# Kernel optimization log

Hardware: AMD Instinct MI355X
Metric: run time of the kernel (lower is better)

Reference implementation:

```python
import jax, jax.numpy as jnp
import numpy as np

EMBED_DIM = 1024
NUM_HEADS = 16
HEAD_DIM = EMBED_DIM // NUM_HEADS


def setup_inputs() -> dict:
    key = jax.random.key(0)
    ks = jax.random.split(key, 10)
    s = 1.0 / np.sqrt(EMBED_DIM)
    x = jax.random.normal(ks[0], (4, 2048, EMBED_DIM), dtype=jnp.float32)
    return {
        "x": x,
        "Wq": jax.random.normal(ks[1], (EMBED_DIM, EMBED_DIM), jnp.float32) * s,
        "bq": jnp.zeros((EMBED_DIM,), jnp.float32),
        "Wk": jax.random.normal(ks[2], (EMBED_DIM, EMBED_DIM), jnp.float32) * s,
        "bk": jnp.zeros((EMBED_DIM,), jnp.float32),
        "Wv": jax.random.normal(ks[3], (EMBED_DIM, EMBED_DIM), jnp.float32) * s,
        "bv": jnp.zeros((EMBED_DIM,), jnp.float32),
        "Wo": jax.random.normal(ks[4], (EMBED_DIM, EMBED_DIM), jnp.float32) * s,
        "bo": jnp.zeros((EMBED_DIM,), jnp.float32),
        "head_scaling": jnp.ones((NUM_HEADS,), jnp.float32),
    }


def reference(x, Wq, bq, Wk, bk, Wv, bv, Wo, bo, head_scaling):
    B, S, E = x.shape
    H, D = NUM_HEADS, HEAD_DIM
    scale = 1.0 / np.sqrt(D)
    # projections (torch Linear: y = x @ W.T + b)
    q = (x @ Wq.T + bq).reshape(B, S, H, D).transpose(0, 2, 1, 3)  # [B,H,S,D]
    k = (x @ Wk.T + bk).reshape(B, S, H, D).transpose(0, 2, 1, 3)
    v = (x @ Wv.T + bv).reshape(B, S, H, D).transpose(0, 2, 1, 3)
    scores = jnp.einsum("bhqd,bhkd->bhqk", q, k) * scale
    attn = jax.nn.softmax(scores, axis=-1)
    head_imp = jax.nn.softmax(head_scaling)[None, :, None, None]  # [1,H,1,1]
    attn = attn * head_imp
    out = jnp.einsum("bhqk,bhkd->bhqd", attn, v)
    out = out.transpose(0, 2, 1, 3).reshape(B, S, E)
    return out @ Wo.T + bo
```

## Files before the change

### kernel.cpp

```cpp
#include <hip/hip_runtime.h>

typedef __bf16 bf16x8 __attribute__((ext_vector_type(8)));
typedef float f32x4 __attribute__((ext_vector_type(4)));
typedef unsigned short ushort8v __attribute__((ext_vector_type(8)));

constexpr int E = 1024;
constexpr int T = 8192;
constexpr size_t TE  = (size_t)T * E;
constexpr size_t WSZ = (size_t)E * E;

#define QSCALE 0.18033688011112042f

__device__ __forceinline__ unsigned short f2bf(float f) {
    union { float f; unsigned int i; } x; x.f = f;
    unsigned int i = x.i;
    return (unsigned short)((i + 0x7fffu + ((i >> 16) & 1u)) >> 16);
}

__device__ __forceinline__ void gload16(const unsigned short* g, unsigned short* l) {
    __builtin_amdgcn_global_load_lds(
        (const __attribute__((address_space(1))) unsigned int*)g,
        (__attribute__((address_space(3))) unsigned int*)l, 16, 0, 0);
}

__global__ __launch_bounds__(256)
void cvt_kernel(const float* __restrict__ x,
                const float* __restrict__ w0, const float* __restrict__ w1,
                const float* __restrict__ w2, const float* __restrict__ w3,
                unsigned short* __restrict__ xb, unsigned short* __restrict__ wb)
{
    size_t i = ((size_t)blockIdx.x * 256 + threadIdx.x) * 8;
    const float* src;
    unsigned short* dst;
    if (i < TE) { src = x + i; dst = xb + i; }
    else {
        size_t j = i - TE;
        int w = (int)(j >> 20);
        size_t off = j & (WSZ - 1);
        src = (w == 0 ? w0 : w == 1 ? w1 : w == 2 ? w2 : w3) + off;
        dst = wb + ((size_t)w << 20) + off;
    }
    float4 a = *(const float4*)src;
    float4 b = *(const float4*)(src + 4);
    union { unsigned short u[8]; uint4 v; } p;
    p.u[0] = f2bf(a.x); p.u[1] = f2bf(a.y); p.u[2] = f2bf(a.z); p.u[3] = f2bf(a.w);
    p.u[4] = f2bf(b.x); p.u[5] = f2bf(b.y); p.u[6] = f2bf(b.z); p.u[7] = f2bf(b.w);
    *(uint4*)dst = p.v;
}

template <int MODE>
__device__ __forceinline__ void gemm_body(const unsigned short* __restrict__ X,
                                          const unsigned short* __restrict__ W,
                                          const float* __restrict__ bias,
                                          void* __restrict__ outp, int t0, int n0,
                                          float oscale)
{
    __shared__ unsigned short As[128 * 32];
    __shared__ unsigned short Bs[128 * 32];

    const int tid  = threadIdx.x;
    const int wave = tid >> 6;
    const int lane = tid & 63;
    const int quad = lane >> 4;
    const int l16  = lane & 15;
    const int wm   = wave >> 1;
    const int wn   = wave & 1;
    const int ldr  = lane >> 2;
    const int ldc  = (lane & 3) ^ ((lane >> 3) & 3);
    const int fsw  = (l16 >> 1) & 3;

    f32x4 acc[4][4];
#pragma unroll
    for (int i = 0; i < 4; i++)
#pragma unroll
        for (int j = 0; j < 4; j++)
            acc[i][j] = (f32x4){0.f, 0.f, 0.f, 0.f};

    for (int k0 = 0; k0 < E; k0 += 32) {
#pragma unroll
        for (int n = 0; n < 2; n++) {
            const int row = wave * 32 + n * 16;
            gload16(&X[(size_t)(t0 + row + ldr) * E + k0 + ldc * 8], &As[row * 32 + lane * 8]);
            gload16(&W[(size_t)(n0 + row + ldr) * E + k0 + ldc * 8], &Bs[row * 32 + lane * 8]);
        }
        __syncthreads();

        bf16x8 af[4], bfr[4];
#pragma unroll
        for (int i = 0; i < 4; i++)
            af[i] = *(const bf16x8*)&As[(wm * 64 + i * 16 + l16) * 32 + (quad ^ fsw) * 8];
#pragma unroll
        for (int j = 0; j < 4; j++)
            bfr[j] = *(const bf16x8*)&Bs[(wn * 64 + j * 16 + l16) * 32 + (quad ^ fsw) * 8];

#pragma unroll
        for (int i = 0; i < 4; i++)
#pragma unroll
            for (int j = 0; j < 4; j++) {
                if (MODE == 2)
                    acc[i][j] = __builtin_amdgcn_mfma_f32_16x16x32_bf16(af[i], bfr[j], acc[i][j], 0, 0, 0);
                else
                    acc[i][j] = __builtin_amdgcn_mfma_f32_16x16x32_bf16(bfr[j], af[i], acc[i][j], 0, 0, 0);
            }
        __syncthreads();
    }

    if (MODE == 2) {
#pragma unroll
        for (int j = 0; j < 4; j++) {
            const int gc = n0 + wn * 64 + j * 16 + l16;
            const float bj = bias[gc];
#pragma unroll
            for (int i = 0; i < 4; i++) {
                const int gr0 = t0 + wm * 64 + i * 16 + quad * 4;
                union { unsigned short u[4]; uint2 v; } o;
#pragma unroll
                for (int r = 0; r < 4; r++) o.u[r] = f2bf((acc[i][j][r] + bj) * oscale);
                unsigned short* vt = (unsigned short*)outp;
                *(uint2*)&vt[((size_t)((gr0 >> 11) * 16 + (gc >> 6)) * 64 + (gc & 63)) * 2048 + (gr0 & 2047)] = o.v;
            }
        }
    } else {
#pragma unroll
        for (int j = 0; j < 4; j++) {
            const int nb = n0 + wn * 64 + j * 16 + quad * 4;
            const float4 b4 = *(const float4*)&bias[nb];
#pragma unroll
            for (int i = 0; i < 4; i++) {
                const int t = t0 + wm * 64 + i * 16 + l16;
                if (MODE == 1) {
                    float4 o;
                    o.x = (acc[i][j][0] + b4.x) * oscale;
                    o.y = (acc[i][j][1] + b4.y) * oscale;
                    o.z = (acc[i][j][2] + b4.z) * oscale;
                    o.w = (acc[i][j][3] + b4.w) * oscale;
                    *(float4*)&((float*)outp)[(size_t)t * E + nb] = o;
                } else {
                    union { unsigned short u[4]; uint2 v; } o;
                    o.u[0] = f2bf((acc[i][j][0] + b4.x) * oscale);
                    o.u[1] = f2bf((acc[i][j][1] + b4.y) * oscale);
                    o.u[2] = f2bf((acc[i][j][2] + b4.z) * oscale);
                    o.u[3] = f2bf((acc[i][j][3] + b4.w) * oscale);
                    *(uint2*)&((unsigned short*)outp)[(size_t)t * E + nb] = o.v;
                }
            }
        }
    }
}

__global__ __launch_bounds__(256)
void gemm_qkv(const unsigned short* __restrict__ Xb, const unsigned short* __restrict__ Wb,
              const float* __restrict__ bq, const float* __restrict__ bk, const float* __restrict__ bv,
              unsigned short* __restrict__ Qb, unsigned short* __restrict__ Kb, unsigned short* __restrict__ VTb)
{
    const int t0 = blockIdx.x * 128;
    const int y = blockIdx.y;
    const int seg = y >> 3;
    const int n0 = (y & 7) * 128;
    const unsigned short* W = Wb + (size_t)seg * WSZ;
    if (seg == 0)      gemm_body<0>(Xb, W, bq, Qb,  t0, n0, QSCALE);
    else if (seg == 1) gemm_body<0>(Xb, W, bk, Kb,  t0, n0, 1.0f);
    else               gemm_body<2>(Xb, W, bv, VTb, t0, n0, 1.0f);
}

__global__ __launch_bounds__(256)
void gemm_out(const unsigned short* __restrict__ AOb, const unsigned short* __restrict__ Wob,
              const float* __restrict__ bo, float* __restrict__ out)
{
    gemm_body<1>(AOb, Wob, bo, out, blockIdx.x * 128, blockIdx.y * 128, 1.0f);
}

__global__ __launch_bounds__(256, 8)
void attn_kernel(const unsigned short* __restrict__ Q,
                 const unsigned short* __restrict__ K,
                 const unsigned short* __restrict__ VT,
                 const float* __restrict__ hs,
                 unsigned short* __restrict__ AO)
{
    constexpr int S = 2048, H = 16;
    const int hb = blockIdx.x;
    const int qt = blockIdx.y;
    const int h  = hb >> 2;
    const int b  = hb & 3;

    const int tid  = threadIdx.x;
    const int wave = tid >> 6;
    const int lane = tid & 63;
    const int quad = lane >> 4;
    const int l16  = lane & 15;

    __shared__ unsigned short Kpl[2][2 * 32 * 32];
    __shared__ unsigned short Vpl[2][64 * 32];
    __shared__ unsigned short Pt[4][16 * 32];

    float mx = -1e30f;
    for (int i = 0; i < H; i++) mx = fmaxf(mx, hs[i]);
    float ss = 0.f;
    for (int i = 0; i < H; i++) ss += __expf(hs[i] - mx);
    const float head_imp = __expf(hs[h] - mx) / ss;

    const int base_t  = b * S;
    const int colbase = h * 64;
    const int q0 = qt * 64 + wave * 16;

    bf16x8 qf[2];
#pragma unroll
    for (int c = 0; c < 2; c++)
        qf[c] = *(const bf16x8*)&Q[(size_t)(base_t + q0 + l16) * E + colbase + c * 32 + quad * 8];

    f32x4 oT[4];
#pragma unroll
    for (int t = 0; t < 4; t++) oT[t] = (f32x4){0.f, 0.f, 0.f, 0.f};
    f32x4 l4 = (f32x4){0.f, 0.f, 0.f, 0.f};

    const int sc   = (lane & 3) ^ ((lane >> 3) & 3);
    const int krow = (tid >> 2) & 31;
    const int kch  = tid >> 7;
    const int vrow = tid >> 2;
    const int fsw  = (l16 >> 1) & 3;
    const unsigned short* const vbase = VT + (size_t)(b * 16 + h) * 64 * 2048;
    unsigned short* const myP = &Pt[wave][0];

    auto stage = [&](int kt, int bu) {
        const int kbase = base_t + kt * 32;
        gload16(&K[(size_t)(kbase + krow) * E + colbase + kch * 32 + sc * 8], &Kpl[bu][tid * 8]);
        gload16(&vbase[(size_t)vrow * 2048 + kt * 32 + sc * 8], &Vpl[bu][tid * 8]);
    };

    stage(0, 0);

    for (int kt = 0; kt < 64; kt++) {
        __syncthreads();
        if (kt < 63) stage(kt + 1, (kt + 1) & 1);
        const int cb = kt & 1;

        bf16x8 kf[2][2], vf[4];
#pragma unroll
        for (int tk = 0; tk < 2; tk++)
#pragma unroll
            for (int ch = 0; ch < 2; ch++)
                kf[tk][ch] = *(const bf16x8*)&Kpl[cb][ch * 1024 + (tk * 16 + l16) * 32 + (quad ^ fsw) * 8];
#pragma unroll
        for (int tau = 0; tau < 4; tau++)
            vf[tau] = *(const bf16x8*)&Vpl[cb][(tau * 16 + l16) * 32 + (quad ^ fsw) * 8];

#pragma unroll
        for (int tk = 0; tk < 2; tk++) {
            f32x4 st = (f32x4){0.f, 0.f, 0.f, 0.f};
            st = __builtin_amdgcn_mfma_f32_16x16x32_bf16(kf[tk][0], qf[0], st, 0, 0, 0);
            st = __builtin_amdgcn_mfma_f32_16x16x32_bf16(kf[tk][1], qf[1], st, 0, 0, 0);
            float p0 = __builtin_amdgcn_exp2f(st[0]);
            float p1 = __builtin_amdgcn_exp2f(st[1]);
            float p2 = __builtin_amdgcn_exp2f(st[2]);
            float p3 = __builtin_amdgcn_exp2f(st[3]);
            l4[0] += p0; l4[1] += p1; l4[2] += p2; l4[3] += p3;
            uint2 pk;
            pk.x = __builtin_amdgcn_perm(
                __builtin_bit_cast(unsigned int, p1), __builtin_bit_cast(unsigned int, p0), 0x07060302u);
            pk.y = __builtin_amdgcn_perm(
                __builtin_bit_cast(unsigned int, p3), __builtin_bit_cast(unsigned int, p2), 0x07060302u);
            const int u = (tk * 4 + quad) ^ (2 * fsw);
            *(uint2*)&myP[l16 * 32 + u * 4] = pk;
        }

        asm volatile("" ::: "memory");

        ushort8v pu = *(const ushort8v*)&myP[l16 * 32 + (quad ^ fsw) * 8];

#pragma unroll
        for (int tau = 0; tau < 4; tau++)
            oT[tau] = __builtin_amdgcn_mfma_f32_16x16x32_bf16(
                vf[tau], __builtin_bit_cast(bf16x8, pu), oT[tau], 0, 0, 0);
    }

    float l = l4[0] + l4[1] + l4[2] + l4[3];
    l += __shfl_xor(l, 16);
    l += __shfl_xor(l, 32);
    const float inv = head_imp / l;

#pragma unroll
    for (int tau = 0; tau < 4; tau++) {
        union { unsigned short u[4]; uint2 v; } o;
#pragma unroll
        for (int r = 0; r < 4; r++) o.u[r] = f2bf(oT[tau][r] * inv);
        *(uint2*)&AO[(size_t)(base_t + q0 + l16) * E + colbase + tau * 16 + quad * 4] = o.v;
    }
}

extern "C" void kernel_launch(void* const* d_in, const int* in_sizes, int n_in,
                              void* d_out, int out_size, void* d_ws, size_t ws_size,
                              hipStream_t stream)
{
    const float* x  = (const float*)d_in[0];
    const float* Wq = (const float*)d_in[1];
    const float* bq = (const float*)d_in[2];
    const float* Wk = (const float*)d_in[3];
    const float* bk = (const float*)d_in[4];
    const float* Wv = (const float*)d_in[5];
    const float* bv = (const float*)d_in[6];
    const float* Wo = (const float*)d_in[7];
    const float* bo = (const float*)d_in[8];
    const float* hs = (const float*)d_in[9];
    float* out = (float*)d_out;

    unsigned short* ws = (unsigned short*)d_ws;
    unsigned short* xb  = ws;
    unsigned short* wb  = ws + TE;
    unsigned short* Qb  = ws + TE + 4 * WSZ;
    unsigned short* AOb = Qb + TE;
    unsigned short* Kb  = (unsigned short*)d_out;
    unsigned short* VTb = Kb + TE;

    dim3 bb(256, 1, 1);
    hipLaunchKernelGGL(cvt_kernel, dim3(6144, 1, 1), bb, 0, stream, x, Wq, Wk, Wv, Wo, xb, wb);
    hipLaunchKernelGGL(gemm_qkv, dim3(64, 24, 1), bb, 0, stream, xb, wb, bq, bk, bv, Qb, Kb, VTb);
    hipLaunchKernelGGL(attn_kernel, dim3(64, 32, 1), bb, 0, stream, Qb, Kb, VTb, hs, AOb);
    hipLaunchKernelGGL(gemm_out, dim3(64, 8, 1), bb, 0, stream, AOb, wb + 3 * WSZ, bo, out);
}
```

Before: 310.9 us.

## Double per-wave query tile and transpose P in registers with permlane swaps

Each attention wave now processes two 16-row query tiles (128 queries per block, half the grid), so every K and V fragment read from LDS feeds twice as many MFMAs. The probability matrix is no longer written to and re-read from a per-wave LDS buffer. It is rearranged into the B-operand layout with permlane32/permlane16 swaps instead. This raises register pressure, so launch bounds are relaxed to 4 blocks per SM, and the halved grid gives fewer blocks for latency hiding.

```diff
diff --git a/kernel.cpp b/kernel.cpp
--- a/kernel.cpp
+++ b/kernel.cpp
@@ -2,7 +2,6 @@
 
 typedef __bf16 bf16x8 __attribute__((ext_vector_type(8)));
 typedef float f32x4 __attribute__((ext_vector_type(4)));
-typedef unsigned short ushort8v __attribute__((ext_vector_type(8)));
 
 constexpr int E = 1024;
 constexpr int T = 8192;
@@ -15,6 +14,12 @@
     union { float f; unsigned int i; } x; x.f = f;
     unsigned int i = x.i;
     return (unsigned short)((i + 0x7fffu + ((i >> 16) & 1u)) >> 16);
+}
+
+__device__ __forceinline__ unsigned int pack_rtz(float lo, float hi) {
+    return __builtin_amdgcn_perm(
+        __builtin_bit_cast(unsigned int, hi),
+        __builtin_bit_cast(unsigned int, lo), 0x07060302u);
 }
 
 __device__ __forceinline__ void gload16(const unsigned short* g, unsigned short* l) {
@@ -170,7 +175,7 @@
     gemm_body<1>(AOb, Wob, bo, out, blockIdx.x * 128, blockIdx.y * 128, 1.0f);
 }
 
-__global__ __launch_bounds__(256, 8)
+__global__ __launch_bounds__(256, 4)
 void attn_kernel(const unsigned short* __restrict__ Q,
                  const unsigned short* __restrict__ K,
                  const unsigned short* __restrict__ VT,
@@ -191,7 +196,6 @@
 
     __shared__ unsigned short Kpl[2][2 * 32 * 32];
     __shared__ unsigned short Vpl[2][64 * 32];
-    __shared__ unsigned short Pt[4][16 * 32];
 
     float mx = -1e30f;
     for (int i = 0; i < H; i++) mx = fmaxf(mx, hs[i]);
@@ -201,17 +205,23 @@
 
     const int base_t  = b * S;
     const int colbase = h * 64;
-    const int q0 = qt * 64 + wave * 16;
-
-    bf16x8 qf[2];
-#pragma unroll
-    for (int c = 0; c < 2; c++)
-        qf[c] = *(const bf16x8*)&Q[(size_t)(base_t + q0 + l16) * E + colbase + c * 32 + quad * 8];
-
-    f32x4 oT[4];
-#pragma unroll
-    for (int t = 0; t < 4; t++) oT[t] = (f32x4){0.f, 0.f, 0.f, 0.f};
-    f32x4 l4 = (f32x4){0.f, 0.f, 0.f, 0.f};
+    const int q0 = qt * 128 + wave * 32;
+
+    bf16x8 qf[2][2];
+#pragma unroll
+    for (int qi = 0; qi < 2; qi++)
+#pragma unroll
+        for (int c = 0; c < 2; c++)
+            qf[qi][c] = *(const bf16x8*)&Q[(size_t)(base_t + q0 + qi * 16 + l16) * E + colbase + c * 32 + quad * 8];
+
+    f32x4 oT[2][4];
+#pragma unroll
+    for (int qi = 0; qi < 2; qi++)
+#pragma unroll
+        for (int t = 0; t < 4; t++) oT[qi][t] = (f32x4){0.f, 0.f, 0.f, 0.f};
+    f32x4 l4[2];
+    l4[0] = (f32x4){0.f, 0.f, 0.f, 0.f};
+    l4[1] = (f32x4){0.f, 0.f, 0.f, 0.f};
 
     const int sc   = (lane & 3) ^ ((lane >> 3) & 3);
     const int krow = (tid >> 2) & 31;
@@ -219,7 +229,6 @@
     const int vrow = tid >> 2;
     const int fsw  = (l16 >> 1) & 3;
     const unsigned short* const vbase = VT + (size_t)(b * 16 + h) * 64 * 2048;
-    unsigned short* const myP = &Pt[wave][0];
 
     auto stage = [&](int kt, int bu) {
         const int kbase = base_t + kt * 32;
@@ -234,56 +243,66 @@
         if (kt < 63) stage(kt + 1, (kt + 1) & 1);
         const int cb = kt & 1;
 
-        bf16x8 kf[2][2], vf[4];
+        bf16x8 kf[2][2];
 #pragma unroll
         for (int tk = 0; tk < 2; tk++)
 #pragma unroll
             for (int ch = 0; ch < 2; ch++)
                 kf[tk][ch] = *(const bf16x8*)&Kpl[cb][ch * 1024 + (tk * 16 + l16) * 32 + (quad ^ fsw) * 8];
-#pragma unroll
-        for (int tau = 0; tau < 4; tau++)
-            vf[tau] = *(const bf16x8*)&Vpl[cb][(tau * 16 + l16) * 32 + (quad ^ fsw) * 8];
-
-#pragma unroll
-        for (int tk = 0; tk < 2; tk++) {
-            f32x4 st = (f32x4){0.f, 0.f, 0.f, 0.f};
-            st = __builtin_amdgcn_mfma_f32_16x16x32_bf16(kf[tk][0], qf[0], st, 0, 0, 0);
-            st = __builtin_amdgcn_mfma_f32_16x16x32_bf16(kf[tk][1], qf[1], st, 0, 0, 0);
-            float p0 = __builtin_amdgcn_exp2f(st[0]);
-            float p1 = __builtin_amdgcn_exp2f(st[1]);
-            float p2 = __builtin_amdgcn_exp2f(st[2]);
-            float p3 = __builtin_amdgcn_exp2f(st[3]);
-            l4[0] += p0; l4[1] += p1; l4[2] += p2; l4[3] += p3;
-            uint2 pk;
-            pk.x = __builtin_amdgcn_perm(
-                __builtin_bit_cast(unsigned int, p1), __builtin_bit_cast(unsigned int, p0), 0x07060302u);
-            pk.y = __builtin_amdgcn_perm(
-                __builtin_bit_cast(unsigned int, p3), __builtin_bit_cast(unsigned int, p2), 0x07060302u);
-            const int u = (tk * 4 + quad) ^ (2 * fsw);
-            *(uint2*)&myP[l16 * 32 + u * 4] = pk;
-        }
-
-        asm volatile("" ::: "memory");
-
-        ushort8v pu = *(const ushort8v*)&myP[l16 * 32 + (quad ^ fsw) * 8];
-
-#pragma unroll
-        for (int tau = 0; tau < 4; tau++)
-            oT[tau] = __builtin_amdgcn_mfma_f32_16x16x32_bf16(
-                vf[tau], __builtin_bit_cast(bf16x8, pu), oT[tau], 0, 0, 0);
-    }
-
-    float l = l4[0] + l4[1] + l4[2] + l4[3];
-    l += __shfl_xor(l, 16);
-    l += __shfl_xor(l, 32);
-    const float inv = head_imp / l;
-
-#pragma unroll
-    for (int tau = 0; tau < 4; tau++) {
-        union { unsigned short u[4]; uint2 v; } o;
-#pragma unroll
-        for (int r = 0; r < 4; r++) o.u[r] = f2bf(oT[tau][r] * inv);
-        *(uint2*)&AO[(size_t)(base_t + q0 + l16) * E + colbase + tau * 16 + quad * 4] = o.v;
+
+        unsigned int pbw[2][4];
+#pragma unroll
+        for (int qi = 0; qi < 2; qi++) {
+            unsigned int pw[4];
+#pragma unroll
+            for (int tk = 0; tk < 2; tk++) {
+                f32x4 st = (f32x4){0.f, 0.f, 0.f, 0.f};
+                st = __builtin_amdgcn_mfma_f32_16x16x32_bf16(kf[tk][0], qf[qi][0], st, 0, 0, 0);
+                st = __builtin_amdgcn_mfma_f32_16x16x32_bf16(kf[tk][1], qf[qi][1], st, 0, 0, 0);
+                float p0 = __builtin_amdgcn_exp2f(st[0]);
+                float p1 = __builtin_amdgcn_exp2f(st[1]);
+                float p2 = __builtin_amdgcn_exp2f(st[2]);
+                float p3 = __builtin_amdgcn_exp2f(st[3]);
+                l4[qi][0] += p0; l4[qi][1] += p1; l4[qi][2] += p2; l4[qi][3] += p3;
+                pw[tk * 2 + 0] = pack_rtz(p0, p1);
+                pw[tk * 2 + 1] = pack_rtz(p2, p3);
+            }
+            auto s1 = __builtin_amdgcn_permlane32_swap(pw[0], pw[2], false, false);
+            auto s2 = __builtin_amdgcn_permlane32_swap(pw[1], pw[3], false, false);
+            auto t1 = __builtin_amdgcn_permlane16_swap(s1[0], s1[1], false, false);
+            auto t2 = __builtin_amdgcn_permlane16_swap(s2[0], s2[1], false, false);
+            pbw[qi][0] = t1[0];
+            pbw[qi][1] = t2[0];
+            pbw[qi][2] = t1[1];
+            pbw[qi][3] = t2[1];
+        }
+
+#pragma unroll
+        for (int tau = 0; tau < 4; tau++) {
+            bf16x8 vf = *(const bf16x8*)&Vpl[cb][(tau * 16 + l16) * 32 + (quad ^ fsw) * 8];
+#pragma unroll
+            for (int qi = 0; qi < 2; qi++) {
+                union { unsigned int w[4]; bf16x8 v; } pb;
+                pb.w[0] = pbw[qi][0]; pb.w[1] = pbw[qi][1];
+                pb.w[2] = pbw[qi][2]; pb.w[3] = pbw[qi][3];
+                oT[qi][tau] = __builtin_amdgcn_mfma_f32_16x16x32_bf16(vf, pb.v, oT[qi][tau], 0, 0, 0);
+            }
+        }
+    }
+
+#pragma unroll
+    for (int qi = 0; qi < 2; qi++) {
+        float l = l4[qi][0] + l4[qi][1] + l4[qi][2] + l4[qi][3];
+        l += __shfl_xor(l, 16);
+        l += __shfl_xor(l, 32);
+        const float inv = head_imp / l;
+#pragma unroll
+        for (int tau = 0; tau < 4; tau++) {
+            union { unsigned short u[4]; uint2 v; } o;
+#pragma unroll
+            for (int r = 0; r < 4; r++) o.u[r] = f2bf(oT[qi][tau][r] * inv);
+            *(uint2*)&AO[(size_t)(base_t + q0 + qi * 16 + l16) * E + colbase + tau * 16 + quad * 4] = o.v;
+        }
     }
 }
 
@@ -314,6 +333,6 @@
     dim3 bb(256, 1, 1);
     hipLaunchKernelGGL(cvt_kernel, dim3(6144, 1, 1), bb, 0, stream, x, Wq, Wk, Wv, Wo, xb, wb);
     hipLaunchKernelGGL(gemm_qkv, dim3(64, 24, 1), bb, 0, stream, xb, wb, bq, bk, bv, Qb, Kb, VTb);
-    hipLaunchKernelGGL(attn_kernel, dim3(64, 32, 1), bb, 0, stream, Qb, Kb, VTb, hs, AOb);
+    hipLaunchKernelGGL(attn_kernel, dim3(64, 16, 1), bb, 0, stream, Qb, Kb, VTb, hs, AOb);
     hipLaunchKernelGGL(gemm_out, dim3(64, 8, 1), bb, 0, stream, AOb, wb + 3 * WSZ, bo, out);
 }
```

Result: faster. 282.8 us (-9.0%).
